# Kernel optimization log

Measured on AMD Instinct MI355X. Metric: run time of the kernel, lower is better.

## Reference

```python
import jax, jax.numpy as jnp
import numpy as np
import math

DIM = 1024
HEADS = 16
PAIR_DIM = 64
POOL = 4  # seq_len // pair_len = 2048 // 512


def central_mask_features(P, feature_size=64):
    half = feature_size // 2
    rel_pos = jnp.arange(2 * P - 1) - (P - 1)                       # [2P-1]
    # torch.logspace(0, log10(P - half + 1), half) == 10**linspace
    widths = jnp.arange(half) + 10.0 ** jnp.linspace(0.0, math.log10(P - half + 1), half)
    emb = (widths[None, :] > rel_pos[:, None]).astype(jnp.float32)  # [2P-1, half]
    signed = jnp.sign(rel_pos)[:, None].astype(jnp.float32) * emb
    return jnp.concatenate([emb, signed], axis=-1)                  # [2P-1, 64]


def relative_shift(x):
    # Faithful replication of the torch pad/view/slice sequence.
    B, P, L, H = x.shape  # L == 2P-1
    x = jnp.pad(x, ((0, 0), (1, 0), (0, 0), (0, 0)))  # [B, P+1, L, H]
    x = x.reshape(B, P + 1, L, H)[:, 1:]              # [B, P, L, H]
    return x[:, :, :P]                                # [B, P, P, H]


def setup_inputs() -> dict:
    key = jax.random.key(0)
    ks = jax.random.split(key, 12)
    HC = HEADS * PAIR_DIM
    s = lambda n: 1.0 / math.sqrt(n)
    return {
        "x": jax.random.normal(ks[0], (4, 2048, DIM), dtype=jnp.float32),
        "Wq": jax.random.normal(ks[1], (HC, DIM), dtype=jnp.float32) * s(DIM),
        "Wk": jax.random.normal(ks[2], (HC, DIM), dtype=jnp.float32) * s(DIM),
        "Wpos": jax.random.normal(ks[3], (HC, 64), dtype=jnp.float32) * s(64),
        "bpos": jax.random.normal(ks[4], (HC,), dtype=jnp.float32) * 0.01,
        "q_bias": jnp.zeros((1, 1, HEADS, PAIR_DIM), dtype=jnp.float32),
        "k_bias": jnp.zeros((1, 1, HEADS, PAIR_DIM), dtype=jnp.float32),
        "Wout": jax.random.normal(ks[5], (PAIR_DIM, HEADS), dtype=jnp.float32) * s(HEADS),
        "bout": jax.random.normal(ks[6], (PAIR_DIM,), dtype=jnp.float32) * 0.01,
        "Wyq": jax.random.normal(ks[7], (PAIR_DIM, DIM), dtype=jnp.float32) * s(DIM),
        "Wyk": jax.random.normal(ks[8], (PAIR_DIM, DIM), dtype=jnp.float32) * s(DIM),
    }


def reference(x, Wq, Wk, Wpos, bpos, q_bias, k_bias, Wout, bout, Wyq, Wyk):
    B, S, D = x.shape
    # AvgPool1d(kernel=stride=POOL) over the sequence dim
    x_ds = x.reshape(B, S // POOL, POOL, D).mean(axis=2)   # [B, P, D]
    P = x_ds.shape[1]
    q = (x_ds @ Wq.T).reshape(B, P, HEADS, PAIR_DIM)
    k = (x_ds @ Wk.T).reshape(B, P, HEADS, PAIR_DIM)
    pos_feat = central_mask_features(P, 64)                 # [2P-1, 64]
    pos_enc = (pos_feat @ Wpos.T + bpos).reshape(2 * P - 1, HEADS, PAIR_DIM)
    rel_q_a = relative_shift(jnp.einsum('bqhc,phc->bqph', q + q_bias, pos_enc))
    rel_k_a = relative_shift(jnp.einsum('bkhc,phc->bkph', k + k_bias, pos_enc))
    dot = jnp.einsum('bqhc,bkhc->bqkh', q, k)               # [B, P, P, H]
    a = dot + (rel_q_a + jnp.transpose(rel_k_a, (0, 2, 1, 3))) * 0.5
    g = jax.nn.gelu(x_ds, approximate=False)                # torch F.gelu exact
    yq = g @ Wyq.T                                          # [B, P, PAIR_DIM]
    yk = g @ Wyk.T
    pair = a @ Wout.T + bout + yq[:, :, None, :] + yk[:, None, :, :]
    return pair                                             # [B, P, P, PAIR_DIM]
```

## Files before the change

### kernel.cpp

```cpp
#include <hip/hip_runtime.h>
#include <math.h>


typedef unsigned short u16;
typedef unsigned int   u32;
typedef __attribute__((ext_vector_type(8)))  short short8;
typedef __attribute__((ext_vector_type(16))) float float16;

#define SEQ 2048
#define DIMN 1024

__device__ __forceinline__ u16 f2bf(float f) {
    union { float f; u32 u; } v; v.f = f;
    u32 r = v.u + 0x7fffu + ((v.u >> 16) & 1u);
    return (u16)(r >> 16);
}
__device__ __forceinline__ float bf2f(u16 h) {
    union { u32 u; float f; } v; v.u = ((u32)h) << 16;
    return v.f;
}
__device__ __forceinline__ void ld_g2l16(u16* lds, const u16* g) {
    __builtin_amdgcn_global_load_lds((const __attribute__((address_space(1))) u32*)g,
                                     (__attribute__((address_space(3))) u32*)lds, 16, 0, 0);
}

struct alignas(8) us4 { u16 x, y, z, w; };

__global__ __launch_bounds__(256) void k_prep(
    const float* __restrict__ x,
    const float* __restrict__ Wq, const float* __restrict__ Wk,
    const float* __restrict__ Wyq, const float* __restrict__ Wyk,
    const float* __restrict__ Wpos, const float* __restrict__ bpos,
    u16* __restrict__ xds, u16* __restrict__ g,
    u16* __restrict__ wqb, u16* __restrict__ wkb,
    u16* __restrict__ wyqb, u16* __restrict__ wykb,
    float* __restrict__ peA, float* __restrict__ peD)
{
    int bk = blockIdx.x, tid = threadIdx.x;
    if (bk < 1024) {
        int i = (bk * 256 + tid) * 4;
        float4 a = *(const float4*)(Wq + i);
        us4 o; o.x=f2bf(a.x); o.y=f2bf(a.y); o.z=f2bf(a.z); o.w=f2bf(a.w);
        *(us4*)(wqb + i) = o;
        a = *(const float4*)(Wk + i);
        o.x=f2bf(a.x); o.y=f2bf(a.y); o.z=f2bf(a.z); o.w=f2bf(a.w);
        *(us4*)(wkb + i) = o;
        if (i < 65536) {
            a = *(const float4*)(Wyq + i);
            o.x=f2bf(a.x); o.y=f2bf(a.y); o.z=f2bf(a.z); o.w=f2bf(a.w);
            *(us4*)(wyqb + i) = o;
            a = *(const float4*)(Wyk + i);
            o.x=f2bf(a.x); o.y=f2bf(a.y); o.z=f2bf(a.z); o.w=f2bf(a.w);
            *(us4*)(wykb + i) = o;
        }
    } else if (bk < 3072) {
        int r = bk - 1024;
        int d4 = tid * 4;
        int b = r >> 9, p = r & 511;
        const float* base = x + ((size_t)(b * SEQ + p * 4)) * DIMN + d4;
        float4 a0 = *(const float4*)(base);
        float4 a1 = *(const float4*)(base + DIMN);
        float4 a2 = *(const float4*)(base + 2 * DIMN);
        float4 a3 = *(const float4*)(base + 3 * DIMN);
        float m0=(a0.x+a1.x+a2.x+a3.x)*0.25f, m1=(a0.y+a1.y+a2.y+a3.y)*0.25f;
        float m2=(a0.z+a1.z+a2.z+a3.z)*0.25f, m3=(a0.w+a1.w+a2.w+a3.w)*0.25f;
        size_t o = (size_t)r * DIMN + d4;
        us4 xo; xo.x=f2bf(m0); xo.y=f2bf(m1); xo.z=f2bf(m2); xo.w=f2bf(m3);
        *(us4*)(xds + o) = xo;
        const float is2 = 0.70710678118654752f;
        us4 go;
        go.x = f2bf(0.5f*m0*(1.f+erff(m0*is2)));
        go.y = f2bf(0.5f*m1*(1.f+erff(m1*is2)));
        go.z = f2bf(0.5f*m2*(1.f+erff(m2*is2)));
        go.w = f2bf(0.5f*m3*(1.f+erff(m3*is2)));
        *(us4*)(g + o) = go;
    } else {
        int t = (bk - 3072) * 256 + tid;
        if (t < 1024) {
            const float* wr = Wpos + t * 64;
            float s1 = 0.f, s2 = 0.f;
            for (int m = 0; m < 32; m++)  s1 += wr[m];
            for (int m = 32; m < 64; m++) s2 += wr[m];
            peA[t] = s1 - s2 + bpos[t];
            peD[t] = s2;
        }
    }
}

__global__ __launch_bounds__(256) void k_gemm(
    const u16* __restrict__ xds, const u16* __restrict__ g,
    const u16* __restrict__ wqb, const u16* __restrict__ wkb,
    const u16* __restrict__ wyqb, const u16* __restrict__ wykb,
    u16* __restrict__ qA, u16* __restrict__ kB,
    float* __restrict__ yqlin, float* __restrict__ yklin)
{
    __shared__ alignas(16) u16 Al[128 * 32];
    __shared__ alignas(16) u16 Bl[64 * 32];
    int nt = blockIdx.x, mt = blockIdx.y;
    const u16* Asrc; const u16* Wsrc; int col0; int mode;
    if (nt < 16)       { Asrc = xds; Wsrc = wqb;  col0 = nt * 64;        mode = 0; }
    else if (nt < 32)  { Asrc = xds; Wsrc = wkb;  col0 = (nt - 16) * 64; mode = 1; }
    else if (nt == 32) { Asrc = g;   Wsrc = wyqb; col0 = 0;              mode = 2; }
    else               { Asrc = g;   Wsrc = wykb; col0 = 0;              mode = 3; }
    int r0 = mt * 128;
    int tid = threadIdx.x;
    int wv = tid >> 6, ln = tid & 63;
    int lane31 = ln & 31, half = ln >> 5;
    float16 acc0, acc1;
#pragma unroll
    for (int e = 0; e < 16; e++) { acc0[e] = 0.f; acc1[e] = 0.f; }
    int row_l = wv * 32 + lane31;
    int swzA = (row_l >> 1) & 3;
    int colL0 = lane31, colL1 = 32 + lane31;
    int swzB0 = (colL0 >> 1) & 3, swzB1 = (colL1 >> 1) & 3;

    for (int k0 = 0; k0 < 1024; k0 += 32) {
#pragma unroll
        for (int q = 0; q < 2; q++) {
            int n = q * 256 + wv * 64 + ln;
            int row = n >> 2, ccs = n & 3;
            int cc = ccs ^ ((row >> 1) & 3);
            ld_g2l16(Al + (size_t)(q * 256 + wv * 64) * 8,
                     Asrc + (size_t)(r0 + row) * 1024 + k0 + cc * 8);
        }
        {
            int n = wv * 64 + ln;
            int row = n >> 2, ccs = n & 3;
            int cc = ccs ^ ((row >> 1) & 3);
            ld_g2l16(Bl + (size_t)(wv * 64) * 8,
                     Wsrc + (size_t)(col0 + row) * 1024 + k0 + cc * 8);
        }
        __syncthreads();
        short8 a0  = *(const short8*)(Al + (row_l * 4 + ((0 + half) ^ swzA)) * 8);
        short8 a1  = *(const short8*)(Al + (row_l * 4 + ((2 + half) ^ swzA)) * 8);
        short8 b00 = *(const short8*)(Bl + (colL0 * 4 + ((0 + half) ^ swzB0)) * 8);
        short8 b01 = *(const short8*)(Bl + (colL0 * 4 + ((2 + half) ^ swzB0)) * 8);
        short8 b10 = *(const short8*)(Bl + (colL1 * 4 + ((0 + half) ^ swzB1)) * 8);
        short8 b11 = *(const short8*)(Bl + (colL1 * 4 + ((2 + half) ^ swzB1)) * 8);
        acc0 = __builtin_amdgcn_mfma_f32_32x32x16_bf16(a0, b00, acc0, 0, 0, 0);
        acc0 = __builtin_amdgcn_mfma_f32_32x32x16_bf16(a1, b01, acc0, 0, 0, 0);
        acc1 = __builtin_amdgcn_mfma_f32_32x32x16_bf16(a0, b10, acc1, 0, 0, 0);
        acc1 = __builtin_amdgcn_mfma_f32_32x32x16_bf16(a1, b11, acc1, 0, 0, 0);
        __syncthreads();
    }
#pragma unroll
    for (int ct = 0; ct < 2; ct++) {
#pragma unroll
        for (int reg = 0; reg < 16; reg++) {
            float v = ct ? acc1[reg] : acc0[reg];
            int rowp = (reg & 3) + 8 * (reg >> 2) + 4 * half;
            int r = r0 + wv * 32 + rowp;
            int col = col0 + ct * 32 + lane31;
            if (mode <= 1) {
                int bb = r >> 9, ii = r & 511;
                int h = col >> 6, c = col & 63;
                size_t chunk = ((size_t)((bb * 16 + h) * 8 + (c >> 3))) * 512 + ii;
                u16* dst = (mode == 0) ? qA : kB;
                dst[chunk * 8 + (c & 7)] = f2bf(v);
            } else {
                float* dst = (mode == 2) ? yqlin : yklin;
                dst[(size_t)r * 64 + col] = v;
            }
        }
    }
}

__global__ __launch_bounds__(64) void k_uv(
    const u16* __restrict__ qA, const u16* __restrict__ kB,
    const float* __restrict__ yqlin, const float* __restrict__ yklin,
    const float* __restrict__ peA, const float* __restrict__ peD,
    const float* __restrict__ qbias, const float* __restrict__ kbias,
    const float* __restrict__ Wout, const float* __restrict__ bout,
    float* __restrict__ U, float* __restrict__ V,
    float* __restrict__ dU, float* __restrict__ dV)
{
    __shared__ float qrow[1024], krow[1024];
    __shared__ float RA[4][16];
    int r = blockIdx.x; int b = r >> 9, i = r & 511;
    int t = threadIdx.x;
#pragma unroll
    for (int u = 0; u < 2; u++) {
        int cidx = t * 2 + u;
        int h = cidx >> 3, sub = cidx & 7;
        size_t chunk = ((size_t)((b * 16 + h) * 8 + sub)) * 512 + i;
        const u16* sq = qA + chunk * 8;
        const u16* sk = kB + chunk * 8;
        int c0 = h * 64 + sub * 8;
#pragma unroll
        for (int e = 0; e < 8; e++) { qrow[c0 + e] = bf2f(sq[e]); krow[c0 + e] = bf2f(sk[e]); }
    }
    __syncthreads();
    {
        int h = t & 15, which = t >> 4;
        const float* rw = (which < 2) ? qrow : krow;
        const float* bs = (which < 2) ? qbias : kbias;
        const float* pe = (which & 1) ? peD : peA;
        float s = 0.f;
        for (int c = 0; c < 64; c++) s += (rw[h * 64 + c] + bs[h * 64 + c]) * pe[h * 64 + c];
        RA[which][h] = s;
    }
    __syncthreads();
    int d = t;
    float uA = 0.f, uD = 0.f, vA = 0.f, vD = 0.f;
#pragma unroll
    for (int hh = 0; hh < 16; hh++) {
        float w = Wout[d * 16 + hh];
        uA += RA[0][hh] * w; uD += RA[1][hh] * w;
        vA += RA[2][hh] * w; vD += RA[3][hh] * w;
    }
    size_t o = (size_t)r * 64 + d;
    U[o]  = yqlin[o] + 0.5f * uA + bout[d];
    dU[o] = 0.5f * uD;
    V[o]  = yklin[o] + 0.5f * vA;
    dV[o] = 0.5f * vD;
}

__global__ __launch_bounds__(256) void k_main(
    const u16* __restrict__ qA, const u16* __restrict__ kB,
    const float* __restrict__ Wout,
    const float* __restrict__ U, const float* __restrict__ V,
    float* __restrict__ out)
{
    __shared__ alignas(16) u16 Asm[1024 * 20];
    int jt = blockIdx.x, it = blockIdx.y, b = blockIdx.z;
    int i0 = it * 32, j0 = jt * 32;
    int tid = threadIdx.x, wv = tid >> 6, ln = tid & 63;
    int lane31 = ln & 31, half = ln >> 5;

    float16 acc[4];
#pragma unroll
    for (int hh = 0; hh < 4; hh++) {
        int h = wv * 4 + hh;
        size_t hbase = ((size_t)(b * 16 + h)) * 8;
        short8 qa[4], kb4[4];
#pragma unroll
        for (int ks = 0; ks < 4; ks++) {
            size_t ch = (hbase + ks * 2 + half) * 512;
            qa[ks]  = *(const short8*)(qA + (ch + i0 + lane31) * 8);
            kb4[ks] = *(const short8*)(kB + (ch + j0 + lane31) * 8);
        }
        float16 a;
#pragma unroll
        for (int e = 0; e < 16; e++) a[e] = 0.f;
#pragma unroll
        for (int ks = 0; ks < 4; ks++)
            a = __builtin_amdgcn_mfma_f32_32x32x16_bf16(qa[ks], kb4[ks], a, 0, 0, 0);
        acc[hh] = a;
    }
#pragma unroll
    for (int reg = 0; reg < 16; reg++) {
        int row = (reg & 3) + 8 * (reg >> 2) + 4 * half;
        int pos = row * 32 + lane31;
        u32 pk0 = (u32)f2bf(acc[0][reg]) | ((u32)f2bf(acc[1][reg]) << 16);
        u32 pk1 = (u32)f2bf(acc[2][reg]) | ((u32)f2bf(acc[3][reg]) << 16);
        u32* bp = (u32*)(Asm + pos * 20 + wv * 4);
        bp[0] = pk0; bp[1] = pk1;
    }
    short8 wfr[2];
#pragma unroll
    for (int dt = 0; dt < 2; dt++) {
        const float* wp = Wout + (dt * 32 + lane31) * 16 + half * 8;
        float4 w0 = *(const float4*)(wp);
        float4 w1 = *(const float4*)(wp + 4);
        short8 t8;
        t8[0]=(short)f2bf(w0.x); t8[1]=(short)f2bf(w0.y); t8[2]=(short)f2bf(w0.z); t8[3]=(short)f2bf(w0.w);
        t8[4]=(short)f2bf(w1.x); t8[5]=(short)f2bf(w1.y); t8[6]=(short)f2bf(w1.z); t8[7]=(short)f2bf(w1.w);
        wfr[dt] = t8;
    }
    float vreg[2][16];
#pragma unroll
    for (int dt = 0; dt < 2; dt++)
#pragma unroll
        for (int reg = 0; reg < 16; reg++) {
            int row = (reg & 3) + 8 * (reg >> 2) + 4 * half;
            vreg[dt][reg] = V[((size_t)(b * 512 + j0 + row)) * 64 + dt * 32 + lane31];
        }
    __syncthreads();
    for (int m = 0; m < 8; m++) {
        int il = wv * 8 + m;
        const u16* ap = Asm + (il * 32 + lane31) * 20 + half * 8;
        union { short8 v; uint2 q[2]; } au;
        au.q[0] = *(const uint2*)(ap);
        au.q[1] = *(const uint2*)(ap + 4);
        int ig = i0 + il;
        size_t rowbase = (size_t)(b * 512 + ig);
#pragma unroll
        for (int dt = 0; dt < 2; dt++) {
            float16 z;
#pragma unroll
            for (int e = 0; e < 16; e++) z[e] = 0.f;
            float16 pa = __builtin_amdgcn_mfma_f32_32x32x16_bf16(au.v, wfr[dt], z, 0, 0, 0);
            float uval = U[rowbase * 64 + dt * 32 + lane31];
            float* ob = out + (rowbase * 512 + j0) * 64 + dt * 32 + lane31;
#pragma unroll
            for (int reg = 0; reg < 16; reg++) {
                int row = (reg & 3) + 8 * (reg >> 2) + 4 * half;
                ob[(size_t)row * 64] = pa[reg] + uval + vreg[dt][reg];
            }
        }
    }
}

__global__ __launch_bounds__(256) void k_edge(
    const float* __restrict__ dU, const float* __restrict__ dV, float* __restrict__ out)
{
    int t = blockIdx.x * 256 + threadIdx.x;
    int side = t >> 17;
    int rem = t & 131071;
    int b = rem >> 15;
    int r = (rem >> 6) & 511;
    int d = rem & 63;
    if (side == 0) {
        size_t o = (((size_t)(b * 512 + r)) * 512 + 511) * 64 + d;
        float add = dU[((size_t)(b * 512 + r)) * 64 + d];
        if (r == 511) add += dV[((size_t)(b * 512 + 511)) * 64 + d];
        out[o] += add;
    } else if (r != 511) {
        size_t o = (((size_t)(b * 512 + 511)) * 512 + r) * 64 + d;
        out[o] += dV[((size_t)(b * 512 + r)) * 64 + d];
    }
}

extern "C" void kernel_launch(void* const* d_in, const int* in_sizes, int n_in,
                              void* d_out, int out_size, void* d_ws, size_t ws_size,
                              hipStream_t stream)
{
    const float* x    = (const float*)d_in[0];
    const float* Wq   = (const float*)d_in[1];
    const float* Wk   = (const float*)d_in[2];
    const float* Wpos = (const float*)d_in[3];
    const float* bpos = (const float*)d_in[4];
    const float* qb   = (const float*)d_in[5];
    const float* kb   = (const float*)d_in[6];
    const float* Wout = (const float*)d_in[7];
    const float* bout = (const float*)d_in[8];
    const float* Wyq  = (const float*)d_in[9];
    const float* Wyk  = (const float*)d_in[10];
    float* out = (float*)d_out;
    char* w = (char*)d_ws;
    u16* xds   = (u16*)(w + 0);
    u16* g     = (u16*)(w + 4194304);
    u16* wqb   = (u16*)(w + 8388608);
    u16* wkb   = (u16*)(w + 10485760);
    u16* wyqb  = (u16*)(w + 12582912);
    u16* wykb  = (u16*)(w + 12713984);
    u16* qA    = (u16*)(w + 12845056);
    u16* kB2   = (u16*)(w + 17039360);
    float* yqlin = (float*)(w + 21233664);
    float* yklin = (float*)(w + 21757952);
    float* peA   = (float*)(w + 22282240);
    float* peD   = (float*)(w + 22286336);
    float* U     = (float*)(w + 22290432);
    float* V     = (float*)(w + 22814720);
    float* dU    = (float*)(w + 23339008);
    float* dV    = (float*)(w + 23863296);

    k_prep<<<dim3(3076), dim3(256), 0, stream>>>(x, Wq, Wk, Wyq, Wyk, Wpos, bpos,
                                                 xds, g, wqb, wkb, wyqb, wykb, peA, peD);
    k_gemm<<<dim3(34, 16), dim3(256), 0, stream>>>(xds, g, wqb, wkb, wyqb, wykb,
                                                   qA, kB2, yqlin, yklin);
    k_uv<<<dim3(2048), dim3(64), 0, stream>>>(qA, kB2, yqlin, yklin, peA, peD,
                                              qb, kb, Wout, bout, U, V, dU, dV);
    k_main<<<dim3(16, 16, 4), dim3(256), 0, stream>>>(qA, kB2, Wout, U, V, out);
    k_edge<<<dim3(1024), dim3(256), 0, stream>>>(dU, dV, out);
}
```

Before: 369.2 us.

## Share A tile across q/k GEMMs, fold edge fixups into main kernel, nontemporal stores

The projection GEMM now computes the q and k outputs (or yq and yk) in the same block, so each A tile is loaded once for two weight matrices. This halves the grid and the A-operand traffic, at the cost of more accumulator registers per thread. The separate edge kernel, which did read-modify-write on the last row and column of the output, is removed. Its dU/dV additions are now applied inside k_main before the store, and the main output stores use nontemporal hints to reduce cache pollution from the large output write.

```diff
diff --git a/kernel.cpp b/kernel.cpp
--- a/kernel.cpp
+++ b/kernel.cpp
@@ -95,20 +95,19 @@
     float* __restrict__ yqlin, float* __restrict__ yklin)
 {
     __shared__ alignas(16) u16 Al[128 * 32];
-    __shared__ alignas(16) u16 Bl[64 * 32];
+    __shared__ alignas(16) u16 B0l[64 * 32];
+    __shared__ alignas(16) u16 B1l[64 * 32];
     int nt = blockIdx.x, mt = blockIdx.y;
-    const u16* Asrc; const u16* Wsrc; int col0; int mode;
-    if (nt < 16)       { Asrc = xds; Wsrc = wqb;  col0 = nt * 64;        mode = 0; }
-    else if (nt < 32)  { Asrc = xds; Wsrc = wkb;  col0 = (nt - 16) * 64; mode = 1; }
-    else if (nt == 32) { Asrc = g;   Wsrc = wyqb; col0 = 0;              mode = 2; }
-    else               { Asrc = g;   Wsrc = wykb; col0 = 0;              mode = 3; }
+    const u16 *Asrc, *W0, *W1; int col0; int mode;
+    if (nt < 16) { Asrc = xds; W0 = wqb;  W1 = wkb;  col0 = nt * 64; mode = 0; }
+    else         { Asrc = g;   W0 = wyqb; W1 = wykb; col0 = 0;       mode = 1; }
     int r0 = mt * 128;
     int tid = threadIdx.x;
     int wv = tid >> 6, ln = tid & 63;
     int lane31 = ln & 31, half = ln >> 5;
-    float16 acc0, acc1;
-#pragma unroll
-    for (int e = 0; e < 16; e++) { acc0[e] = 0.f; acc1[e] = 0.f; }
+    float16 aq0, aq1, ak0, ak1;
+#pragma unroll
+    for (int e = 0; e < 16; e++) { aq0[e]=0.f; aq1[e]=0.f; ak0[e]=0.f; ak1[e]=0.f; }
     int row_l = wv * 32 + lane31;
     int swzA = (row_l >> 1) & 3;
     int colL0 = lane31, colL1 = 32 + lane31;
@@ -127,38 +126,51 @@
             int n = wv * 64 + ln;
             int row = n >> 2, ccs = n & 3;
             int cc = ccs ^ ((row >> 1) & 3);
-            ld_g2l16(Bl + (size_t)(wv * 64) * 8,
-                     Wsrc + (size_t)(col0 + row) * 1024 + k0 + cc * 8);
+            ld_g2l16(B0l + (size_t)(wv * 64) * 8,
+                     W0 + (size_t)(col0 + row) * 1024 + k0 + cc * 8);
+            ld_g2l16(B1l + (size_t)(wv * 64) * 8,
+                     W1 + (size_t)(col0 + row) * 1024 + k0 + cc * 8);
         }
         __syncthreads();
         short8 a0  = *(const short8*)(Al + (row_l * 4 + ((0 + half) ^ swzA)) * 8);
         short8 a1  = *(const short8*)(Al + (row_l * 4 + ((2 + half) ^ swzA)) * 8);
-        short8 b00 = *(const short8*)(Bl + (colL0 * 4 + ((0 + half) ^ swzB0)) * 8);
-        short8 b01 = *(const short8*)(Bl + (colL0 * 4 + ((2 + half) ^ swzB0)) * 8);
-        short8 b10 = *(const short8*)(Bl + (colL1 * 4 + ((0 + half) ^ swzB1)) * 8);
-        short8 b11 = *(const short8*)(Bl + (colL1 * 4 + ((2 + half) ^ swzB1)) * 8);
-        acc0 = __builtin_amdgcn_mfma_f32_32x32x16_bf16(a0, b00, acc0, 0, 0, 0);
-        acc0 = __builtin_amdgcn_mfma_f32_32x32x16_bf16(a1, b01, acc0, 0, 0, 0);
-        acc1 = __builtin_amdgcn_mfma_f32_32x32x16_bf16(a0, b10, acc1, 0, 0, 0);
-        acc1 = __builtin_amdgcn_mfma_f32_32x32x16_bf16(a1, b11, acc1, 0, 0, 0);
+        short8 q00 = *(const short8*)(B0l + (colL0 * 4 + ((0 + half) ^ swzB0)) * 8);
+        short8 q01 = *(const short8*)(B0l + (colL0 * 4 + ((2 + half) ^ swzB0)) * 8);
+        short8 q10 = *(const short8*)(B0l + (colL1 * 4 + ((0 + half) ^ swzB1)) * 8);
+        short8 q11 = *(const short8*)(B0l + (colL1 * 4 + ((2 + half) ^ swzB1)) * 8);
+        short8 k00 = *(const short8*)(B1l + (colL0 * 4 + ((0 + half) ^ swzB0)) * 8);
+        short8 k01 = *(const short8*)(B1l + (colL0 * 4 + ((2 + half) ^ swzB0)) * 8);
+        short8 k10 = *(const short8*)(B1l + (colL1 * 4 + ((0 + half) ^ swzB1)) * 8);
+        short8 k11 = *(const short8*)(B1l + (colL1 * 4 + ((2 + half) ^ swzB1)) * 8);
+        aq0 = __builtin_amdgcn_mfma_f32_32x32x16_bf16(a0, q00, aq0, 0, 0, 0);
+        aq0 = __builtin_amdgcn_mfma_f32_32x32x16_bf16(a1, q01, aq0, 0, 0, 0);
+        aq1 = __builtin_amdgcn_mfma_f32_32x32x16_bf16(a0, q10, aq1, 0, 0, 0);
+        aq1 = __builtin_amdgcn_mfma_f32_32x32x16_bf16(a1, q11, aq1, 0, 0, 0);
+        ak0 = __builtin_amdgcn_mfma_f32_32x32x16_bf16(a0, k00, ak0, 0, 0, 0);
+        ak0 = __builtin_amdgcn_mfma_f32_32x32x16_bf16(a1, k01, ak0, 0, 0, 0);
+        ak1 = __builtin_amdgcn_mfma_f32_32x32x16_bf16(a0, k10, ak1, 0, 0, 0);
+        ak1 = __builtin_amdgcn_mfma_f32_32x32x16_bf16(a1, k11, ak1, 0, 0, 0);
         __syncthreads();
     }
 #pragma unroll
-    for (int ct = 0; ct < 2; ct++) {
+    for (int sel = 0; sel < 4; sel++) {
+        int ct = sel & 1;
+        bool isq = (sel < 2);
 #pragma unroll
         for (int reg = 0; reg < 16; reg++) {
-            float v = ct ? acc1[reg] : acc0[reg];
+            float v = (sel == 0) ? aq0[reg] : (sel == 1) ? aq1[reg]
+                    : (sel == 2) ? ak0[reg] : ak1[reg];
             int rowp = (reg & 3) + 8 * (reg >> 2) + 4 * half;
             int r = r0 + wv * 32 + rowp;
             int col = col0 + ct * 32 + lane31;
-            if (mode <= 1) {
+            if (mode == 0) {
                 int bb = r >> 9, ii = r & 511;
                 int h = col >> 6, c = col & 63;
                 size_t chunk = ((size_t)((bb * 16 + h) * 8 + (c >> 3))) * 512 + ii;
-                u16* dst = (mode == 0) ? qA : kB;
+                u16* dst = isq ? qA : kB;
                 dst[chunk * 8 + (c & 7)] = f2bf(v);
             } else {
-                float* dst = (mode == 2) ? yqlin : yklin;
+                float* dst = isq ? yqlin : yklin;
                 dst[(size_t)r * 64 + col] = v;
             }
         }
@@ -219,6 +231,7 @@
     const u16* __restrict__ qA, const u16* __restrict__ kB,
     const float* __restrict__ Wout,
     const float* __restrict__ U, const float* __restrict__ V,
+    const float* __restrict__ dU, const float* __restrict__ dV,
     float* __restrict__ out)
 {
     __shared__ alignas(16) u16 Asm[1024 * 20];
@@ -276,6 +289,7 @@
             vreg[dt][reg] = V[((size_t)(b * 512 + j0 + row)) * 64 + dt * 32 + lane31];
         }
     __syncthreads();
+    bool ej_blk = (jt == 15);
     for (int m = 0; m < 8; m++) {
         int il = wv * 8 + m;
         const u16* ap = Asm + (il * 32 + lane31) * 20 + half * 8;
@@ -283,41 +297,29 @@
         au.q[0] = *(const uint2*)(ap);
         au.q[1] = *(const uint2*)(ap + 4);
         int ig = i0 + il;
+        bool ei = (it == 15) && (il == 31);
         size_t rowbase = (size_t)(b * 512 + ig);
+        size_t jbase = (size_t)(b * 512 + j0);
 #pragma unroll
         for (int dt = 0; dt < 2; dt++) {
+            int dcol = dt * 32 + lane31;
             float16 z;
 #pragma unroll
             for (int e = 0; e < 16; e++) z[e] = 0.f;
             float16 pa = __builtin_amdgcn_mfma_f32_32x32x16_bf16(au.v, wfr[dt], z, 0, 0, 0);
-            float uval = U[rowbase * 64 + dt * 32 + lane31];
-            float* ob = out + (rowbase * 512 + j0) * 64 + dt * 32 + lane31;
+            float uval = U[rowbase * 64 + dcol];
+            float duv = 0.f;
+            if (ej_blk && half) duv = dU[rowbase * 64 + dcol];
+            float* ob = out + (rowbase * 512 + j0) * 64 + dcol;
 #pragma unroll
             for (int reg = 0; reg < 16; reg++) {
                 int row = (reg & 3) + 8 * (reg >> 2) + 4 * half;
-                ob[(size_t)row * 64] = pa[reg] + uval + vreg[dt][reg];
+                float v = pa[reg] + uval + vreg[dt][reg];
+                if (ei) v += dV[(jbase + row) * 64 + dcol];
+                if (reg == 15) v += duv;
+                __builtin_nontemporal_store(v, ob + (size_t)row * 64);
             }
         }
-    }
-}
-
-__global__ __launch_bounds__(256) void k_edge(
-    const float* __restrict__ dU, const float* __restrict__ dV, float* __restrict__ out)
-{
-    int t = blockIdx.x * 256 + threadIdx.x;
-    int side = t >> 17;
-    int rem = t & 131071;
-    int b = rem >> 15;
-    int r = (rem >> 6) & 511;
-    int d = rem & 63;
-    if (side == 0) {
-        size_t o = (((size_t)(b * 512 + r)) * 512 + 511) * 64 + d;
-        float add = dU[((size_t)(b * 512 + r)) * 64 + d];
-        if (r == 511) add += dV[((size_t)(b * 512 + 511)) * 64 + d];
-        out[o] += add;
-    } else if (r != 511) {
-        size_t o = (((size_t)(b * 512 + 511)) * 512 + r) * 64 + d;
-        out[o] += dV[((size_t)(b * 512 + r)) * 64 + d];
     }
 }
 
@@ -357,10 +359,9 @@
 
     k_prep<<<dim3(3076), dim3(256), 0, stream>>>(x, Wq, Wk, Wyq, Wyk, Wpos, bpos,
                                                  xds, g, wqb, wkb, wyqb, wykb, peA, peD);
-    k_gemm<<<dim3(34, 16), dim3(256), 0, stream>>>(xds, g, wqb, wkb, wyqb, wykb,
+    k_gemm<<<dim3(17, 16), dim3(256), 0, stream>>>(xds, g, wqb, wkb, wyqb, wykb,
                                                    qA, kB2, yqlin, yklin);
     k_uv<<<dim3(2048), dim3(64), 0, stream>>>(qA, kB2, yqlin, yklin, peA, peD,
                                               qb, kb, Wout, bout, U, V, dU, dV);
-    k_main<<<dim3(16, 16, 4), dim3(256), 0, stream>>>(qA, kB2, Wout, U, V, out);
-    k_edge<<<dim3(1024), dim3(256), 0, stream>>>(dU, dV, out);
-}
+    k_main<<<dim3(16, 16, 4), dim3(256), 0, stream>>>(qA, kB2, Wout, U, V, dU, dV, out);
+}
```

New measurement: 375.3 us. About the same (+1.7%).
